# Performance work log

Measured on AMD Instinct MI355X. Metric: run time of the kernel, lower is better.

The kernel has to match this reference:

```python
import jax, jax.numpy as jnp
import numpy as np

N_NODES = 10000
N_EDGES = 25000
D_FEAT = 128

def setup_inputs() -> dict:
    key = jax.random.key(0)
    k1, k2, k3 = jax.random.split(key, 3)
    x = jax.random.normal(k1, (N_NODES, D_FEAT), dtype=jnp.float32)
    edge_attr = jax.random.normal(k2, (N_EDGES, D_FEAT), dtype=jnp.float32)
    edge_index = jax.random.randint(k3, (2, N_EDGES), 0, N_NODES, dtype=jnp.int64)
    return {"x": x, "edge_attr": edge_attr, "edge_index": edge_index}

def reference(x, edge_attr, edge_index):
    # lg_node_idx: [E, 2] (src, dst) pairs; each original edge becomes a line-graph node
    lg_node_idx = edge_index.T
    # gather endpoint features and average -> [E, d]
    new_x = x[lg_node_idx].mean(axis=1)
    # stack([x, edge_attr], dim=2).mean(dim=2) == elementwise average
    new_x = (new_x + edge_attr) * 0.5
    col0 = lg_node_idx[:, 0]  # src of each edge
    col1 = lg_node_idx[:, 1]  # dst of each edge
    # edge i -> edge j connected iff dst(i) == src(j) and src(i) != dst(j)
    mask = (col1[:, None] == col0[None, :]) & (col0[:, None] != col1[None, :])  # [E, E]
    rows, cols = jnp.nonzero(mask)  # data-dependent size; eager (non-jit) reference
    lg_edge_index = jnp.stack([rows, cols], axis=0)  # [2, E_lg]
    # attr of line-graph edge = feature of shared node's incoming edge's dst entry
    lg_edge_attr_idx = lg_node_idx[rows][:, 1]
    lg_edge_attr = new_x[lg_edge_attr_idx]
    return new_x, lg_edge_index, lg_edge_attr
```

## Files before the change

### kernel.cpp

```cpp
#include <hip/hip_runtime.h>

#define NN 10000
#define NE 25000
#define DF 128
#define SB 256
#define NBLK ((NE + SB - 1) / SB)
#define NEWXB ((NE * 32 + SB - 1) / SB)

__global__ void k_init(int* __restrict__ head, int* __restrict__ gFlag) {
    int tid = blockIdx.x * blockDim.x + threadIdx.x;
    if (tid < NN) head[tid] = -1;
    if (tid < NBLK) gFlag[tid] = 0;
}

__global__ void k_link(const int* __restrict__ c0,
                       int* __restrict__ head, int* __restrict__ nxt) {
    int j = blockIdx.x * blockDim.x + threadIdx.x;
    if (j >= NE) return;
    nxt[j] = atomicExch(&head[c0[j]], j);
}

__global__ __launch_bounds__(SB) void k_scan_newx(const float* __restrict__ x,
                                                  const float* __restrict__ ea,
                                                  const int* __restrict__ c0,
                                                  const int* __restrict__ c1,
                                                  const int* __restrict__ head,
                                                  const int* __restrict__ nxt,
                                                  int* __restrict__ gFlag,
                                                  int* __restrict__ rowStart,
                                                  float* __restrict__ out) {
    int b = blockIdx.x, t = threadIdx.x;

    if (b >= NBLK) {
        int tid = (b - NBLK) * SB + t;
        if (tid >= NE * 32) return;
        int e = tid >> 5, q = tid & 31;
        int u = c0[e], v = c1[e];
        float4 a  = ((const float4*)(x + (size_t)u * DF))[q];
        float4 bb = ((const float4*)(x + (size_t)v * DF))[q];
        float4 c  = ((const float4*)(ea + (size_t)e * DF))[q];
        float4 r;
        r.x = ((a.x + bb.x) * 0.5f + c.x) * 0.5f;
        r.y = ((a.y + bb.y) * 0.5f + c.y) * 0.5f;
        r.z = ((a.z + bb.z) * 0.5f + c.z) * 0.5f;
        r.w = ((a.w + bb.w) * 0.5f + c.w) * 0.5f;
        ((float4*)(out + (size_t)e * DF))[q] = r;
        return;
    }

    __shared__ int sc[SB];
    __shared__ int sr[SB];
    int i = b * SB + t;
    int cnt = 0;
    if (i < NE) {
        int u = c0[i], v = c1[i];
        for (int j = head[v]; j != -1; j = nxt[j])
            if (c1[j] != u) ++cnt;
    }
    sc[t] = cnt;
    __syncthreads();
    for (int off = 1; off < SB; off <<= 1) {
        int add = (t >= off) ? sc[t - off] : 0;
        __syncthreads();
        sc[t] += add;
        __syncthreads();
    }
    int blockSum = sc[SB - 1];
    if (t == 0) atomicExch(&gFlag[b], blockSum + 1);
    int val = 0;
    if (t < b) {
        int v2;
        do { v2 = atomicAdd(&gFlag[t], 0); } while (v2 == 0);
        val = v2 - 1;
    }
    sr[t] = val;
    __syncthreads();
    for (int off = SB / 2; off > 0; off >>= 1) {
        if (t < off) sr[t] += sr[t + off];
        __syncthreads();
    }
    int base = sr[0];
    if (i < NE) rowStart[i] = base + sc[t] - cnt;
    if (b == NBLK - 1 && t == 0) rowStart[NE] = base + blockSum;
}

__global__ void k_emit(const float* __restrict__ newx,
                       const int* __restrict__ c0, const int* __restrict__ c1,
                       const int* __restrict__ head, const int* __restrict__ nxt,
                       const int* __restrict__ rowStart,
                       float* __restrict__ outRows, float* __restrict__ outCols,
                       float* __restrict__ outAttr) {
    int gtid = blockIdx.x * blockDim.x + threadIdx.x;
    int i = gtid >> 6, lane = gtid & 63;
    if (i >= NE) return;
    int base = rowStart[i];
    int cnt  = rowStart[i + 1] - base;
    if (cnt == 0) return;
    int u = c0[i], v = c1[i];

    int myj = -1, B = 0;
    for (int j = head[v]; j != -1; j = nxt[j], ++B)
        if (B == lane) myj = j;

    if (B <= 64) {
        int myc1 = (myj >= 0) ? c1[myj] : -1;
        bool keep = (myj >= 0) && (myc1 != u);
        int rank = 0;
        for (int q = 0; q < B; ++q) {
            int jq = __shfl(myj, q);
            int cq = __shfl(myc1, q);
            if (cq != u && jq < myj) ++rank;
        }
        if (keep) {
            outRows[base + rank] = (float)i;
            outCols[base + rank] = (float)myj;
        }
    } else {
        int pos = 0;
        for (int j = head[v]; j != -1; j = nxt[j], ++pos) {
            if ((pos & 63) != lane) continue;
            if (c1[j] == u) continue;
            int rank = 0;
            for (int j2 = head[v]; j2 != -1; j2 = nxt[j2])
                rank += (c1[j2] != u && j2 < j) ? 1 : 0;
            outRows[base + rank] = (float)i;
            outCols[base + rank] = (float)j;
        }
    }

    float4 val = ((const float4*)(newx + (size_t)v * DF))[lane & 31];
    for (int tt = (lane >> 5); tt < cnt; tt += 2)
        ((float4*)(outAttr + (size_t)(base + tt) * DF))[lane & 31] = val;
}


extern "C" void kernel_launch(void* const* d_in, const int* in_sizes, int n_in,
                              void* d_out, int out_size, void* d_ws, size_t ws_size,
                              hipStream_t stream) {
    const float* x  = (const float*)d_in[0];
    const float* ea = (const float*)d_in[1];
    const int*   ei = (const int*)d_in[2];
    const int* c0 = ei;
    const int* c1 = ei + NE;

    float* out = (float*)d_out;
    int E_lg = (out_size - NE * DF) / (DF + 2);
    if (E_lg < 0) E_lg = 0;

    float* out_newx = out;
    float* out_rows = out + (size_t)NE * DF;
    float* out_cols = out_rows + E_lg;
    float* out_attr = out_cols + E_lg;

    int* ws       = (int*)d_ws;
    int* head     = ws;
    int* nxt      = head + NN;
    int* rowStart = nxt + NE;
    int* gFlag    = rowStart + NE + 1;

    k_init<<<(NN + SB - 1) / SB, SB, 0, stream>>>(head, gFlag);
    k_link<<<(NE + SB - 1) / SB, SB, 0, stream>>>(c0, head, nxt);
    k_scan_newx<<<NBLK + NEWXB, SB, 0, stream>>>(x, ea, c0, c1, head, nxt,
                                                 gFlag, rowStart, out_newx);
    k_emit<<<(NE * 64 + SB - 1) / SB, SB, 0, stream>>>(out_newx, c0, c1, head, nxt,
                                                       rowStart, out_rows, out_cols, out_attr);
}
```

Before: 40.34 us.

## Fuse linked-list build into scan kernel via grid barrier, use nontemporal stores

Merges the k_link kernel into the scan/new_x kernel. The first NBLK blocks build the head/next lists and then wait on a global atomic barrier before counting, which removes one kernel launch. Output stores in the emit kernel become nontemporal stores. The spin barrier depends on all NBLK scan blocks being co-resident; this is likely on this GPU because block indices are dispatched in order, but it is not guaranteed.

```diff
diff --git a/kernel.cpp b/kernel.cpp
--- a/kernel.cpp
+++ b/kernel.cpp
@@ -7,28 +7,26 @@
 #define NBLK ((NE + SB - 1) / SB)
 #define NEWXB ((NE * 32 + SB - 1) / SB)
 
-__global__ void k_init(int* __restrict__ head, int* __restrict__ gFlag) {
+typedef float f4 __attribute__((ext_vector_type(4)));
+
+__global__ void k_init(int* __restrict__ head, int* __restrict__ gFlag,
+                       int* __restrict__ gBar) {
     int tid = blockIdx.x * blockDim.x + threadIdx.x;
     if (tid < NN) head[tid] = -1;
     if (tid < NBLK) gFlag[tid] = 0;
+    if (tid == 0) *gBar = 0;
 }
 
-__global__ void k_link(const int* __restrict__ c0,
-                       int* __restrict__ head, int* __restrict__ nxt) {
-    int j = blockIdx.x * blockDim.x + threadIdx.x;
-    if (j >= NE) return;
-    nxt[j] = atomicExch(&head[c0[j]], j);
-}
-
-__global__ __launch_bounds__(SB) void k_scan_newx(const float* __restrict__ x,
-                                                  const float* __restrict__ ea,
-                                                  const int* __restrict__ c0,
-                                                  const int* __restrict__ c1,
-                                                  const int* __restrict__ head,
-                                                  const int* __restrict__ nxt,
-                                                  int* __restrict__ gFlag,
-                                                  int* __restrict__ rowStart,
-                                                  float* __restrict__ out) {
+__global__ __launch_bounds__(SB) void k_mega(const float* __restrict__ x,
+                                             const float* __restrict__ ea,
+                                             const int* __restrict__ c0,
+                                             const int* __restrict__ c1,
+                                             int* __restrict__ head,
+                                             int* __restrict__ nxt,
+                                             int* __restrict__ gFlag,
+                                             int* __restrict__ gBar,
+                                             int* __restrict__ rowStart,
+                                             float* __restrict__ out) {
     int b = blockIdx.x, t = threadIdx.x;
 
     if (b >= NBLK) {
@@ -48,15 +46,33 @@
         return;
     }
 
-    __shared__ int sc[SB];
-    __shared__ int sr[SB];
     int i = b * SB + t;
+
+    if (i < NE) {
+        int prev = atomicExch(&head[c0[i]], i);
+        __hip_atomic_store(&nxt[i], prev, __ATOMIC_RELAXED, __HIP_MEMORY_SCOPE_AGENT);
+    }
+    __threadfence();
+    __syncthreads();
+    if (t == 0) {
+        atomicAdd(gBar, 1);
+        while (atomicAdd(gBar, 0) < NBLK) __builtin_amdgcn_s_sleep(1);
+    }
+    __syncthreads();
+    __threadfence();
+
     int cnt = 0;
     if (i < NE) {
         int u = c0[i], v = c1[i];
-        for (int j = head[v]; j != -1; j = nxt[j])
+        int j = __hip_atomic_load(&head[v], __ATOMIC_RELAXED, __HIP_MEMORY_SCOPE_AGENT);
+        while (j != -1) {
             if (c1[j] != u) ++cnt;
+            j = __hip_atomic_load(&nxt[j], __ATOMIC_RELAXED, __HIP_MEMORY_SCOPE_AGENT);
+        }
     }
+
+    __shared__ int sc[SB];
+    __shared__ int sr[SB];
     sc[t] = cnt;
     __syncthreads();
     for (int off = 1; off < SB; off <<= 1) {
@@ -112,8 +128,8 @@
             if (cq != u && jq < myj) ++rank;
         }
         if (keep) {
-            outRows[base + rank] = (float)i;
-            outCols[base + rank] = (float)myj;
+            __builtin_nontemporal_store((float)i, &outRows[base + rank]);
+            __builtin_nontemporal_store((float)myj, &outCols[base + rank]);
         }
     } else {
         int pos = 0;
@@ -123,14 +139,15 @@
             int rank = 0;
             for (int j2 = head[v]; j2 != -1; j2 = nxt[j2])
                 rank += (c1[j2] != u && j2 < j) ? 1 : 0;
-            outRows[base + rank] = (float)i;
-            outCols[base + rank] = (float)j;
+            __builtin_nontemporal_store((float)i, &outRows[base + rank]);
+            __builtin_nontemporal_store((float)j, &outCols[base + rank]);
         }
     }
 
-    float4 val = ((const float4*)(newx + (size_t)v * DF))[lane & 31];
+    f4 val = ((const f4*)(newx + (size_t)v * DF))[lane & 31];
     for (int tt = (lane >> 5); tt < cnt; tt += 2)
-        ((float4*)(outAttr + (size_t)(base + tt) * DF))[lane & 31] = val;
+        __builtin_nontemporal_store(val,
+            &((f4*)(outAttr + (size_t)(base + tt) * DF))[lane & 31]);
 }
 
 
@@ -157,11 +174,11 @@
     int* nxt      = head + NN;
     int* rowStart = nxt + NE;
     int* gFlag    = rowStart + NE + 1;
+    int* gBar     = gFlag + NBLK;
 
-    k_init<<<(NN + SB - 1) / SB, SB, 0, stream>>>(head, gFlag);
-    k_link<<<(NE + SB - 1) / SB, SB, 0, stream>>>(c0, head, nxt);
-    k_scan_newx<<<NBLK + NEWXB, SB, 0, stream>>>(x, ea, c0, c1, head, nxt,
-                                                 gFlag, rowStart, out_newx);
+    k_init<<<(NN + SB - 1) / SB, SB, 0, stream>>>(head, gFlag, gBar);
+    k_mega<<<NBLK + NEWXB, SB, 0, stream>>>(x, ea, c0, c1, head, nxt,
+                                            gFlag, gBar, rowStart, out_newx);
     k_emit<<<(NE * 64 + SB - 1) / SB, SB, 0, stream>>>(out_newx, c0, c1, head, nxt,
                                                        rowStart, out_rows, out_cols, out_attr);
 }
```

Result: slower. 66.50 us (+64.8%).

## Fuse scan and emit via decoupled lookback, merge newx into init kernel

Applied to the files above, without the earlier changes.

Moves the new_x computation into the init kernel. The separate scan and emit kernels become one kernel that uses a single-pass decoupled-lookback scan over 64-edge chunks, replacing the serial all-blocks flag wait. Each 1024-thread block counts its chunk, gets its global base and then emits rows, cols and attributes directly, with nontemporal stores. This drops one launch and the rowStart round trip through memory, at the cost of the spin-wait lookback and lower parallelism per chunk during the count phase.

```diff
diff --git a/kernel.cpp b/kernel.cpp
--- a/kernel.cpp
+++ b/kernel.cpp
@@ -4,13 +4,30 @@
 #define NE 25000
 #define DF 128
 #define SB 256
-#define NBLK ((NE + SB - 1) / SB)
-#define NEWXB ((NE * 32 + SB - 1) / SB)
+#define CHUNK 64
+#define NCH ((NE + CHUNK - 1) / CHUNK)
 
-__global__ void k_init(int* __restrict__ head, int* __restrict__ gFlag) {
+typedef float f4 __attribute__((ext_vector_type(4)));
+
+__global__ void k_newx_init(const float* __restrict__ x, const float* __restrict__ ea,
+                            const int* __restrict__ c0, const int* __restrict__ c1,
+                            float* __restrict__ out, int* __restrict__ head,
+                            int* __restrict__ gFlag) {
     int tid = blockIdx.x * blockDim.x + threadIdx.x;
     if (tid < NN) head[tid] = -1;
-    if (tid < NBLK) gFlag[tid] = 0;
+    if (tid < NCH) gFlag[tid] = 0;
+    if (tid >= NE * 32) return;
+    int e = tid >> 5, q = tid & 31;
+    int u = c0[e], v = c1[e];
+    float4 a  = ((const float4*)(x + (size_t)u * DF))[q];
+    float4 bb = ((const float4*)(x + (size_t)v * DF))[q];
+    float4 c  = ((const float4*)(ea + (size_t)e * DF))[q];
+    float4 r;
+    r.x = ((a.x + bb.x) * 0.5f + c.x) * 0.5f;
+    r.y = ((a.y + bb.y) * 0.5f + c.y) * 0.5f;
+    r.z = ((a.z + bb.z) * 0.5f + c.z) * 0.5f;
+    r.w = ((a.w + bb.w) * 0.5f + c.w) * 0.5f;
+    ((float4*)(out + (size_t)e * DF))[q] = r;
 }
 
 __global__ void k_link(const int* __restrict__ c0,
@@ -20,117 +37,121 @@
     nxt[j] = atomicExch(&head[c0[j]], j);
 }
 
-__global__ __launch_bounds__(SB) void k_scan_newx(const float* __restrict__ x,
-                                                  const float* __restrict__ ea,
-                                                  const int* __restrict__ c0,
-                                                  const int* __restrict__ c1,
-                                                  const int* __restrict__ head,
-                                                  const int* __restrict__ nxt,
-                                                  int* __restrict__ gFlag,
-                                                  int* __restrict__ rowStart,
-                                                  float* __restrict__ out) {
+__global__ __launch_bounds__(1024) void k_scan_emit(
+        const float* __restrict__ newx,
+        const int* __restrict__ c0, const int* __restrict__ c1,
+        const int* __restrict__ head, const int* __restrict__ nxt,
+        int* __restrict__ gFlag,
+        float* __restrict__ outRows, float* __restrict__ outCols,
+        float* __restrict__ outAttr) {
+    __shared__ int sCnt[CHUNK];
+    __shared__ int sExc[CHUNK];
+    __shared__ int sBase;
     int b = blockIdx.x, t = threadIdx.x;
+    int wave = t >> 6, lane = t & 63;
+    int e0 = b * CHUNK;
 
-    if (b >= NBLK) {
-        int tid = (b - NBLK) * SB + t;
-        if (tid >= NE * 32) return;
-        int e = tid >> 5, q = tid & 31;
-        int u = c0[e], v = c1[e];
-        float4 a  = ((const float4*)(x + (size_t)u * DF))[q];
-        float4 bb = ((const float4*)(x + (size_t)v * DF))[q];
-        float4 c  = ((const float4*)(ea + (size_t)e * DF))[q];
-        float4 r;
-        r.x = ((a.x + bb.x) * 0.5f + c.x) * 0.5f;
-        r.y = ((a.y + bb.y) * 0.5f + c.y) * 0.5f;
-        r.z = ((a.z + bb.z) * 0.5f + c.z) * 0.5f;
-        r.w = ((a.w + bb.w) * 0.5f + c.w) * 0.5f;
-        ((float4*)(out + (size_t)e * DF))[q] = r;
-        return;
+    if (wave == 0) {
+        int e = e0 + lane;
+        int cnt = 0;
+        if (e < NE) {
+            int u = c0[e], v = c1[e];
+            for (int j = head[v]; j != -1; j = nxt[j])
+                if (c1[j] != u) ++cnt;
+        }
+        int incl = cnt;
+        for (int off = 1; off < 64; off <<= 1) {
+            int vv = __shfl_up(incl, off, 64);
+            if (lane >= off) incl += vv;
+        }
+        int agg = __shfl(incl, 63);
+        sCnt[lane] = cnt;
+        sExc[lane] = incl - cnt;
+        int base = 0;
+        if (b == 0) {
+            if (lane == 0) atomicExch(&gFlag[0], (2 << 30) | agg);
+        } else {
+            if (lane == 0) atomicExch(&gFlag[b], (1 << 30) | agg);
+            int p = b - 1;
+            while (true) {
+                int idx = p - lane;
+                int st, sm;
+                if (idx < 0) { st = 2; sm = 0; }
+                else {
+                    int f;
+                    do {
+                        f = __hip_atomic_load(&gFlag[idx], __ATOMIC_ACQUIRE,
+                                              __HIP_MEMORY_SCOPE_AGENT);
+                        st = (unsigned)f >> 30;
+                    } while (st == 0);
+                    sm = f & 0x3FFFFFFF;
+                }
+                unsigned long long inclMask = __ballot(st == 2);
+                int contrib;
+                if (inclMask) {
+                    int l0 = __ffsll(inclMask) - 1;
+                    contrib = (lane <= l0) ? sm : 0;
+                } else {
+                    contrib = sm;
+                }
+                for (int off = 32; off; off >>= 1)
+                    contrib += __shfl_down(contrib, off, 64);
+                contrib = __shfl(contrib, 0);
+                base += contrib;
+                if (inclMask) break;
+                p -= 64;
+            }
+            if (lane == 0) atomicExch(&gFlag[b], (2 << 30) | (base + agg));
+        }
+        if (lane == 0) sBase = base;
     }
+    __syncthreads();
 
-    __shared__ int sc[SB];
-    __shared__ int sr[SB];
-    int i = b * SB + t;
-    int cnt = 0;
-    if (i < NE) {
+    int gBase = sBase;
+    for (int k = 0; k < 4; ++k) {
+        int el = wave * 4 + k;
+        int i = e0 + el;
+        if (i >= NE) break;
+        int cnt = sCnt[el];
+        if (cnt == 0) continue;
+        int base = gBase + sExc[el];
         int u = c0[i], v = c1[i];
-        for (int j = head[v]; j != -1; j = nxt[j])
-            if (c1[j] != u) ++cnt;
+
+        int myj = -1, B = 0;
+        for (int j = head[v]; j != -1; j = nxt[j], ++B)
+            if (B == lane) myj = j;
+
+        if (B <= 64) {
+            int myc1 = (myj >= 0) ? c1[myj] : -1;
+            bool keep = (myj >= 0) && (myc1 != u);
+            int rank = 0;
+            for (int q = 0; q < B; ++q) {
+                int jq = __shfl(myj, q);
+                int cq = __shfl(myc1, q);
+                if (cq != u && jq < myj) ++rank;
+            }
+            if (keep) {
+                __builtin_nontemporal_store((float)i, &outRows[base + rank]);
+                __builtin_nontemporal_store((float)myj, &outCols[base + rank]);
+            }
+        } else {
+            int pos = 0;
+            for (int j = head[v]; j != -1; j = nxt[j], ++pos) {
+                if ((pos & 63) != lane) continue;
+                if (c1[j] == u) continue;
+                int rank = 0;
+                for (int j2 = head[v]; j2 != -1; j2 = nxt[j2])
+                    rank += (c1[j2] != u && j2 < j) ? 1 : 0;
+                __builtin_nontemporal_store((float)i, &outRows[base + rank]);
+                __builtin_nontemporal_store((float)j, &outCols[base + rank]);
+            }
+        }
+
+        f4 val = ((const f4*)(newx + (size_t)v * DF))[lane & 31];
+        for (int tt = (lane >> 5); tt < cnt; tt += 2)
+            __builtin_nontemporal_store(val,
+                &((f4*)(outAttr + (size_t)(base + tt) * DF))[lane & 31]);
     }
-    sc[t] = cnt;
-    __syncthreads();
-    for (int off = 1; off < SB; off <<= 1) {
-        int add = (t >= off) ? sc[t - off] : 0;
-        __syncthreads();
-        sc[t] += add;
-        __syncthreads();
-    }
-    int blockSum = sc[SB - 1];
-    if (t == 0) atomicExch(&gFlag[b], blockSum + 1);
-    int val = 0;
-    if (t < b) {
-        int v2;
-        do { v2 = atomicAdd(&gFlag[t], 0); } while (v2 == 0);
-        val = v2 - 1;
-    }
-    sr[t] = val;
-    __syncthreads();
-    for (int off = SB / 2; off > 0; off >>= 1) {
-        if (t < off) sr[t] += sr[t + off];
-        __syncthreads();
-    }
-    int base = sr[0];
-    if (i < NE) rowStart[i] = base + sc[t] - cnt;
-    if (b == NBLK - 1 && t == 0) rowStart[NE] = base + blockSum;
-}
-
-__global__ void k_emit(const float* __restrict__ newx,
-                       const int* __restrict__ c0, const int* __restrict__ c1,
-                       const int* __restrict__ head, const int* __restrict__ nxt,
-                       const int* __restrict__ rowStart,
-                       float* __restrict__ outRows, float* __restrict__ outCols,
-                       float* __restrict__ outAttr) {
-    int gtid = blockIdx.x * blockDim.x + threadIdx.x;
-    int i = gtid >> 6, lane = gtid & 63;
-    if (i >= NE) return;
-    int base = rowStart[i];
-    int cnt  = rowStart[i + 1] - base;
-    if (cnt == 0) return;
-    int u = c0[i], v = c1[i];
-
-    int myj = -1, B = 0;
-    for (int j = head[v]; j != -1; j = nxt[j], ++B)
-        if (B == lane) myj = j;
-
-    if (B <= 64) {
-        int myc1 = (myj >= 0) ? c1[myj] : -1;
-        bool keep = (myj >= 0) && (myc1 != u);
-        int rank = 0;
-        for (int q = 0; q < B; ++q) {
-            int jq = __shfl(myj, q);
-            int cq = __shfl(myc1, q);
-            if (cq != u && jq < myj) ++rank;
-        }
-        if (keep) {
-            outRows[base + rank] = (float)i;
-            outCols[base + rank] = (float)myj;
-        }
-    } else {
-        int pos = 0;
-        for (int j = head[v]; j != -1; j = nxt[j], ++pos) {
-            if ((pos & 63) != lane) continue;
-            if (c1[j] == u) continue;
-            int rank = 0;
-            for (int j2 = head[v]; j2 != -1; j2 = nxt[j2])
-                rank += (c1[j2] != u && j2 < j) ? 1 : 0;
-            outRows[base + rank] = (float)i;
-            outCols[base + rank] = (float)j;
-        }
-    }
-
-    float4 val = ((const float4*)(newx + (size_t)v * DF))[lane & 31];
-    for (int tt = (lane >> 5); tt < cnt; tt += 2)
-        ((float4*)(outAttr + (size_t)(base + tt) * DF))[lane & 31] = val;
 }
 
 
@@ -152,16 +173,14 @@
     float* out_cols = out_rows + E_lg;
     float* out_attr = out_cols + E_lg;
 
-    int* ws       = (int*)d_ws;
-    int* head     = ws;
-    int* nxt      = head + NN;
-    int* rowStart = nxt + NE;
-    int* gFlag    = rowStart + NE + 1;
+    int* ws    = (int*)d_ws;
+    int* head  = ws;
+    int* nxt   = head + NN;
+    int* gFlag = nxt + NE;
 
-    k_init<<<(NN + SB - 1) / SB, SB, 0, stream>>>(head, gFlag);
+    k_newx_init<<<(NE * 32 + SB - 1) / SB, SB, 0, stream>>>(x, ea, c0, c1, out_newx,
+                                                            head, gFlag);
     k_link<<<(NE + SB - 1) / SB, SB, 0, stream>>>(c0, head, nxt);
-    k_scan_newx<<<NBLK + NEWXB, SB, 0, stream>>>(x, ea, c0, c1, head, nxt,
-                                                 gFlag, rowStart, out_newx);
-    k_emit<<<(NE * 64 + SB - 1) / SB, SB, 0, stream>>>(out_newx, c0, c1, head, nxt,
-                                                       rowStart, out_rows, out_cols, out_attr);
+    k_scan_emit<<<NCH, 1024, 0, stream>>>(out_newx, c0, c1, head, nxt, gFlag,
+                                          out_rows, out_cols, out_attr);
 }
```

Result: slower. 44.51 us (+10.3%).

## Move new_x computation into emit kernel and recompute attr rows from inputs

Applied to the files above, without the earlier changes.

The new_x elementwise work moves out of the scan kernel and into the emit kernel, so the scan launch only does counting and prefix work. The emit blocks no longer read the new_x output. They recompute the needed row from x and edge_attr, which removes the dependency between the two block types. Output writes now use nontemporal stores to bypass cache retention. The cost is redundant gathers of x and edge_attr for each emitted row.

```diff
diff --git a/kernel.cpp b/kernel.cpp
--- a/kernel.cpp
+++ b/kernel.cpp
@@ -6,6 +6,9 @@
 #define SB 256
 #define NBLK ((NE + SB - 1) / SB)
 #define NEWXB ((NE * 32 + SB - 1) / SB)
+#define EMITB ((NE * 64) / SB)
+
+typedef float f4 __attribute__((ext_vector_type(4)));
 
 __global__ void k_init(int* __restrict__ head, int* __restrict__ gFlag) {
     int tid = blockIdx.x * blockDim.x + threadIdx.x;
@@ -20,36 +23,15 @@
     nxt[j] = atomicExch(&head[c0[j]], j);
 }
 
-__global__ __launch_bounds__(SB) void k_scan_newx(const float* __restrict__ x,
-                                                  const float* __restrict__ ea,
-                                                  const int* __restrict__ c0,
-                                                  const int* __restrict__ c1,
-                                                  const int* __restrict__ head,
-                                                  const int* __restrict__ nxt,
-                                                  int* __restrict__ gFlag,
-                                                  int* __restrict__ rowStart,
-                                                  float* __restrict__ out) {
-    int b = blockIdx.x, t = threadIdx.x;
-
-    if (b >= NBLK) {
-        int tid = (b - NBLK) * SB + t;
-        if (tid >= NE * 32) return;
-        int e = tid >> 5, q = tid & 31;
-        int u = c0[e], v = c1[e];
-        float4 a  = ((const float4*)(x + (size_t)u * DF))[q];
-        float4 bb = ((const float4*)(x + (size_t)v * DF))[q];
-        float4 c  = ((const float4*)(ea + (size_t)e * DF))[q];
-        float4 r;
-        r.x = ((a.x + bb.x) * 0.5f + c.x) * 0.5f;
-        r.y = ((a.y + bb.y) * 0.5f + c.y) * 0.5f;
-        r.z = ((a.z + bb.z) * 0.5f + c.z) * 0.5f;
-        r.w = ((a.w + bb.w) * 0.5f + c.w) * 0.5f;
-        ((float4*)(out + (size_t)e * DF))[q] = r;
-        return;
-    }
-
+__global__ __launch_bounds__(SB) void k_cnt_scan(const int* __restrict__ c0,
+                                                 const int* __restrict__ c1,
+                                                 const int* __restrict__ head,
+                                                 const int* __restrict__ nxt,
+                                                 int* __restrict__ gFlag,
+                                                 int* __restrict__ rowStart) {
     __shared__ int sc[SB];
     __shared__ int sr[SB];
+    int b = blockIdx.x, t = threadIdx.x;
     int i = b * SB + t;
     int cnt = 0;
     if (i < NE) {
@@ -84,13 +66,34 @@
     if (b == NBLK - 1 && t == 0) rowStart[NE] = base + blockSum;
 }
 
-__global__ void k_emit(const float* __restrict__ newx,
-                       const int* __restrict__ c0, const int* __restrict__ c1,
-                       const int* __restrict__ head, const int* __restrict__ nxt,
-                       const int* __restrict__ rowStart,
-                       float* __restrict__ outRows, float* __restrict__ outCols,
-                       float* __restrict__ outAttr) {
-    int gtid = blockIdx.x * blockDim.x + threadIdx.x;
+__global__ __launch_bounds__(SB) void k_emit_newx(
+        const float* __restrict__ x, const float* __restrict__ ea,
+        const int* __restrict__ c0, const int* __restrict__ c1,
+        const int* __restrict__ head, const int* __restrict__ nxt,
+        const int* __restrict__ rowStart,
+        float* __restrict__ outNewx,
+        float* __restrict__ outRows, float* __restrict__ outCols,
+        float* __restrict__ outAttr) {
+    int b = blockIdx.x, t = threadIdx.x;
+
+    if (b < NEWXB) {
+        int tid = b * SB + t;
+        if (tid >= NE * 32) return;
+        int e = tid >> 5, q = tid & 31;
+        int u = c0[e], v = c1[e];
+        float4 a  = ((const float4*)(x + (size_t)u * DF))[q];
+        float4 bb = ((const float4*)(x + (size_t)v * DF))[q];
+        float4 c  = ((const float4*)(ea + (size_t)e * DF))[q];
+        float4 r;
+        r.x = ((a.x + bb.x) * 0.5f + c.x) * 0.5f;
+        r.y = ((a.y + bb.y) * 0.5f + c.y) * 0.5f;
+        r.z = ((a.z + bb.z) * 0.5f + c.z) * 0.5f;
+        r.w = ((a.w + bb.w) * 0.5f + c.w) * 0.5f;
+        ((float4*)(outNewx + (size_t)e * DF))[q] = r;
+        return;
+    }
+
+    int gtid = (b - NEWXB) * SB + t;
     int i = gtid >> 6, lane = gtid & 63;
     if (i >= NE) return;
     int base = rowStart[i];
@@ -112,8 +115,8 @@
             if (cq != u && jq < myj) ++rank;
         }
         if (keep) {
-            outRows[base + rank] = (float)i;
-            outCols[base + rank] = (float)myj;
+            __builtin_nontemporal_store((float)i, &outRows[base + rank]);
+            __builtin_nontemporal_store((float)myj, &outCols[base + rank]);
         }
     } else {
         int pos = 0;
@@ -123,14 +126,19 @@
             int rank = 0;
             for (int j2 = head[v]; j2 != -1; j2 = nxt[j2])
                 rank += (c1[j2] != u && j2 < j) ? 1 : 0;
-            outRows[base + rank] = (float)i;
-            outCols[base + rank] = (float)j;
+            __builtin_nontemporal_store((float)i, &outRows[base + rank]);
+            __builtin_nontemporal_store((float)j, &outCols[base + rank]);
         }
     }
 
-    float4 val = ((const float4*)(newx + (size_t)v * DF))[lane & 31];
+    int vu = c0[v], vv = c1[v];
+    f4 xa = ((const f4*)(x  + (size_t)vu * DF))[lane & 31];
+    f4 xb = ((const f4*)(x  + (size_t)vv * DF))[lane & 31];
+    f4 ec = ((const f4*)(ea + (size_t)v  * DF))[lane & 31];
+    f4 val = ((xa + xb) * 0.5f + ec) * 0.5f;
     for (int tt = (lane >> 5); tt < cnt; tt += 2)
-        ((float4*)(outAttr + (size_t)(base + tt) * DF))[lane & 31] = val;
+        __builtin_nontemporal_store(val,
+            &((f4*)(outAttr + (size_t)(base + tt) * DF))[lane & 31]);
 }
 
 
@@ -160,8 +168,7 @@
 
     k_init<<<(NN + SB - 1) / SB, SB, 0, stream>>>(head, gFlag);
     k_link<<<(NE + SB - 1) / SB, SB, 0, stream>>>(c0, head, nxt);
-    k_scan_newx<<<NBLK + NEWXB, SB, 0, stream>>>(x, ea, c0, c1, head, nxt,
-                                                 gFlag, rowStart, out_newx);
-    k_emit<<<(NE * 64 + SB - 1) / SB, SB, 0, stream>>>(out_newx, c0, c1, head, nxt,
-                                                       rowStart, out_rows, out_cols, out_attr);
+    k_cnt_scan<<<NBLK, SB, 0, stream>>>(c0, c1, head, nxt, gFlag, rowStart);
+    k_emit_newx<<<NEWXB + EMITB, SB, 0, stream>>>(x, ea, c0, c1, head, nxt, rowStart,
+                                                  out_newx, out_rows, out_cols, out_attr);
 }
```

After: 42.31 us. 1.05x slower.
